# Kernel optimization log

Measured on AMD Instinct MI355X. Metric: run time of the kernel, lower is better.

Reference implementation:

```python
import jax, jax.numpy as jnp
import numpy as np

NUM_LEVELS = 4
SEARCH_RADIUS = 4
EPS = 1e-12  # torch F.normalize eps


def _avg_pool2d(x, s):
    # avg pool with kernel=stride=s over last two dims (exact, since H,W divisible by s)
    lead = x.shape[:-2]
    H, W = x.shape[-2], x.shape[-1]
    x = x.reshape(*lead, H // s, s, W // s, s)
    return x.mean(axis=(-3, -1))


def _l2_normalize(x, axis):
    n = jnp.sqrt(jnp.sum(x * x, axis=axis, keepdims=True))
    return x / jnp.maximum(n, EPS)


def _compute_correlation(query, values, radius):
    # query: [B,C,H,W], values: [B,N,C,H,W] -> [B,N,H,W,(2r+1)^2]
    q = _l2_normalize(query, axis=1)
    v = _l2_normalize(values, axis=2)
    corrs = []
    for dy in range(-radius, radius + 1):
        for dx in range(-radius, radius + 1):
            vs = v if (dy == 0 and dx == 0) else jnp.roll(v, (dy, dx), axis=(-2, -1))
            corrs.append(jnp.einsum('bchw,bnchw->bnhw', q, vs))
    return jnp.stack(corrs, axis=-1)


def setup_inputs() -> dict:
    key = jax.random.key(0)
    k1, k2, k3, k4 = jax.random.split(key, 4)
    B, N, C, H, W = 2, 4, 128, 160, 160
    Co = C // 2
    return {
        'query_feat': jax.random.normal(k1, (B, C, H, W), dtype=jnp.float32),
        'value_feats': jax.random.normal(k2, (B, N, C, H, W), dtype=jnp.float32),
        'proj_w': jax.random.normal(k3, (Co, C), dtype=jnp.float32) * (1.0 / np.sqrt(C)),
        'proj_b': jax.random.normal(k4, (Co,), dtype=jnp.float32) * 0.01,
    }


def reference(query_feat, value_feats, proj_w, proj_b):
    # 1x1 conv projection C -> C//2
    q = jnp.einsum('oc,bchw->bohw', proj_w, query_feat) + proj_b[None, :, None, None]
    v = jnp.einsum('oc,bnchw->bnohw', proj_w, value_feats) + proj_b[None, None, :, None, None]
    outs = []
    for level in range(NUM_LEVELS):
        scale = 2 ** level
        radius = max(1, SEARCH_RADIUS // scale)
        if scale > 1:
            q_l = _avg_pool2d(q, scale)
            v_l = _avg_pool2d(v, scale)
        else:
            q_l, v_l = q, v
        outs.append(_compute_correlation(q_l, v_l, radius))
    return tuple(outs)
```

## Files before the change

### kernel.cpp

```cpp
#include <hip/hip_runtime.h>


typedef _Float16 f16;
typedef _Float16 f16x4 __attribute__((ext_vector_type(4)));
typedef _Float16 f16x8 __attribute__((ext_vector_type(8)));
typedef float f32x4 __attribute__((ext_vector_type(4)));

#define EPSN 1e-12f

__global__ __launch_bounds__(256) void prep_weights(
    const float* __restrict__ wt, f16* __restrict__ wh) {
  int gid = blockIdx.x * 256 + threadIdx.x;
  float4 w = *(const float4*)(wt + gid * 4);
  f16x4 h;
  h[0] = (f16)w.x; h[1] = (f16)w.y; h[2] = (f16)w.z; h[3] = (f16)w.w;
  *(f16x4*)(wh + gid * 4) = h;
}

#define LROW 68
#define WS 136

__global__ __launch_bounds__(256, 3) void proj_pool(
    const float* __restrict__ xq, const float* __restrict__ xv,
    const f16* __restrict__ wh, const float* __restrict__ bias,
    f16* __restrict__ h0, f16* __restrict__ h1,
    f16* __restrict__ h2, f16* __restrict__ h3, int P) {
  __shared__ float xs[128 * LROW];
  __shared__ f16 wsh[64 * WS];
  float* accbuf = (float*)wsh;
  float* l3buf = xs;

  int pb = blockIdx.x;
  int bid = (pb & 7) * 500 + (pb >> 3);

  int img = bid / 400;
  int t = bid - img * 400;
  int ty = t / 20, tx = t - ty * 20;
  int py0 = ty * 8, px0 = tx * 8;
  const float* xsrc = (img < 2) ? (xq + (size_t)img * 128 * P)
                                : (xv + (size_t)(img - 2) * 128 * P);

  int tid = threadIdx.x;
  int lane = tid & 63;
  int wv = tid >> 6;
  int cl = lane & 15;
  int quad = lane >> 4;

  for (int m = tid; m < 1024; m += 256) {
    int o = m >> 4, kk = (m & 15) * 8;
    *(f16x8*)(wsh + o * WS + kk) = *(const f16x8*)(wh + o * 128 + kk);
  }

  {
    int cb = tid >> 4;
    int sub = tid & 15;
    int row = sub >> 1, hf = sub & 1;
#pragma unroll
    for (int i = 0; i < 8; ++i) {
      int c = cb + 16 * i;
      float4 v = *(const float4*)(xsrc + (size_t)c * P + (py0 + row) * 160 + px0 + hf * 4);
      int p = row * 8 + hf * 4;
      int x = (p + 8 * ((c >> 3) & 3)) & 63;
      *(float4*)(xs + c * LROW + x) = v;
    }
  }
  __syncthreads();

  f32x4 acc[4];
#pragma unroll
  for (int m = 0; m < 4; ++m) acc[m] = (f32x4)0.f;

  int pxl = wv * 16 + cl;
  int xr = (pxl + 8 * quad) & 63;

#pragma unroll
  for (int kc = 0; kc < 4; ++kc) {
    f16x8 bfr;
#pragma unroll
    for (int k = 0; k < 8; ++k) {
      int c = kc * 32 + quad * 8 + k;
      bfr[k] = (f16)xs[c * LROW + xr];
    }
    f16x8 afr[4];
#pragma unroll
    for (int mt = 0; mt < 4; ++mt)
      afr[mt] = *(const f16x8*)(wsh + (mt * 16 + cl) * WS + kc * 32 + quad * 8);
#pragma unroll
    for (int mt = 0; mt < 4; ++mt)
      acc[mt] = __builtin_amdgcn_mfma_f32_16x16x32_f16(afr[mt], bfr, acc[mt], 0, 0, 0);
  }

  float4 bi[4];
#pragma unroll
  for (int mt = 0; mt < 4; ++mt) bi[mt] = *(const float4*)(bias + mt * 16 + quad * 4);

  __syncthreads();

  float ss = 0.f;
#pragma unroll
  for (int mt = 0; mt < 4; ++mt) {
    acc[mt][0] += bi[mt].x;
    acc[mt][1] += bi[mt].y;
    acc[mt][2] += bi[mt].z;
    acc[mt][3] += bi[mt].w;
    *(float4*)(accbuf + pxl * LROW + mt * 16 + quad * 4) =
        make_float4(acc[mt][0], acc[mt][1], acc[mt][2], acc[mt][3]);
#pragma unroll
    for (int r = 0; r < 4; ++r) ss = fmaf(acc[mt][r], acc[mt][r], ss);
  }
  ss += __shfl_xor(ss, 16, 64);
  ss += __shfl_xor(ss, 32, 64);
  float s = 1.0f / fmaxf(sqrtf(ss), EPSN);
  {
    int gp = (py0 + (pxl >> 3)) * 160 + px0 + (pxl & 7);
    size_t base = ((size_t)img * P + gp) * 64;
#pragma unroll
    for (int mt = 0; mt < 4; ++mt) {
      f16x4 hn;
      hn[0] = (f16)(acc[mt][0] * s);
      hn[1] = (f16)(acc[mt][1] * s);
      hn[2] = (f16)(acc[mt][2] * s);
      hn[3] = (f16)(acc[mt][3] * s);
      *(f16x4*)(h0 + base + mt * 16 + quad * 4) = hn;
    }
  }
  __syncthreads();

  int r2 = wv >> 1, c2 = wv & 1;
  int g = quad, c4 = cl;
  int r1 = 2 * r2 + (g >> 1), c1 = 2 * c2 + (g & 1);
  int p00 = (2 * r1) * 8 + 2 * c1;

  float4 s00 = *(const float4*)(accbuf + p00 * LROW + c4 * 4);
  float4 s01 = *(const float4*)(accbuf + (p00 + 1) * LROW + c4 * 4);
  float4 s10 = *(const float4*)(accbuf + (p00 + 8) * LROW + c4 * 4);
  float4 s11 = *(const float4*)(accbuf + (p00 + 9) * LROW + c4 * 4);
  float4 v1;
  v1.x = 0.25f * (s00.x + s01.x + s10.x + s11.x);
  v1.y = 0.25f * (s00.y + s01.y + s10.y + s11.y);
  v1.z = 0.25f * (s00.z + s01.z + s10.z + s11.z);
  v1.w = 0.25f * (s00.w + s01.w + s10.w + s11.w);

  {
    float s1 = fmaf(v1.x, v1.x, fmaf(v1.y, v1.y, fmaf(v1.z, v1.z, v1.w * v1.w)));
    s1 += __shfl_xor(s1, 1, 64);
    s1 += __shfl_xor(s1, 2, 64);
    s1 += __shfl_xor(s1, 4, 64);
    s1 += __shfl_xor(s1, 8, 64);
    float sc = 1.0f / fmaxf(sqrtf(s1), EPSN);
    f16x4 h;
    h[0] = (f16)(v1.x * sc); h[1] = (f16)(v1.y * sc);
    h[2] = (f16)(v1.z * sc); h[3] = (f16)(v1.w * sc);
    *(f16x4*)(h1 + ((size_t)(img * 80 + ty * 4 + r1) * 80 + tx * 4 + c1) * 64 + c4 * 4) = h;
  }

  float4 q2v;
  q2v.x = v1.x + __shfl_xor(v1.x, 16, 64);
  q2v.y = v1.y + __shfl_xor(v1.y, 16, 64);
  q2v.z = v1.z + __shfl_xor(v1.z, 16, 64);
  q2v.w = v1.w + __shfl_xor(v1.w, 16, 64);
  q2v.x += __shfl_xor(q2v.x, 32, 64);
  q2v.y += __shfl_xor(q2v.y, 32, 64);
  q2v.z += __shfl_xor(q2v.z, 32, 64);
  q2v.w += __shfl_xor(q2v.w, 32, 64);
  q2v.x *= 0.25f; q2v.y *= 0.25f; q2v.z *= 0.25f; q2v.w *= 0.25f;

  {
    float s2 = fmaf(q2v.x, q2v.x, fmaf(q2v.y, q2v.y, fmaf(q2v.z, q2v.z, q2v.w * q2v.w)));
    s2 += __shfl_xor(s2, 1, 64);
    s2 += __shfl_xor(s2, 2, 64);
    s2 += __shfl_xor(s2, 4, 64);
    s2 += __shfl_xor(s2, 8, 64);
    float sc = 1.0f / fmaxf(sqrtf(s2), EPSN);
    if (g == 0) {
      f16x4 h;
      h[0] = (f16)(q2v.x * sc); h[1] = (f16)(q2v.y * sc);
      h[2] = (f16)(q2v.z * sc); h[3] = (f16)(q2v.w * sc);
      *(f16x4*)(h2 + ((size_t)(img * 40 + ty * 2 + r2) * 40 + tx * 2 + c2) * 64 + c4 * 4) = h;
      *(float4*)(l3buf + (wv * 16 + c4) * 4) = q2v;
    }
  }
  __syncthreads();

  if (tid < 16) {
    float4 a0 = *(const float4*)(l3buf + (0 * 16 + tid) * 4);
    float4 a1 = *(const float4*)(l3buf + (1 * 16 + tid) * 4);
    float4 a2 = *(const float4*)(l3buf + (2 * 16 + tid) * 4);
    float4 a3 = *(const float4*)(l3buf + (3 * 16 + tid) * 4);
    float4 q3;
    q3.x = 0.25f * (a0.x + a1.x + a2.x + a3.x);
    q3.y = 0.25f * (a0.y + a1.y + a2.y + a3.y);
    q3.z = 0.25f * (a0.z + a1.z + a2.z + a3.z);
    q3.w = 0.25f * (a0.w + a1.w + a2.w + a3.w);
    float s3 = fmaf(q3.x, q3.x, fmaf(q3.y, q3.y, fmaf(q3.z, q3.z, q3.w * q3.w)));
    s3 += __shfl_xor(s3, 1, 64);
    s3 += __shfl_xor(s3, 2, 64);
    s3 += __shfl_xor(s3, 4, 64);
    s3 += __shfl_xor(s3, 8, 64);
    float sc = 1.0f / fmaxf(sqrtf(s3), EPSN);
    f16x4 h;
    h[0] = (f16)(q3.x * sc); h[1] = (f16)(q3.y * sc);
    h[2] = (f16)(q3.z * sc); h[3] = (f16)(q3.w * sc);
    *(f16x4*)(h3 + ((size_t)(img * 20 + ty) * 20 + tx) * 64 + tid * 4) = h;
  }
}

template <int R>
__device__ __forceinline__ void corr_level(
    const f16* __restrict__ qh, const f16* __restrict__ vh,
    float* __restrict__ out, int H, int W, int T, int blk, float* lw) {
  constexpr int D = 2 * R + 1, DD = D * D;
  constexpr int PS = (DD + 3) & ~3;
  int bn = blk & 7;
  int wv = threadIdx.x >> 6;
  int widx = (blk >> 3) * 4 + wv;
  int h = widx / T;
  int wt = widx - h * T;
  int lane = threadIdx.x & 63;
  int cl = lane & 15, quad = lane >> 4;
  int b = bn >> 2;
  int w0 = wt * 16;
  float* lwv = lw + wv * 16 * PS;

  int ap = w0 + cl; if (ap >= W) ap = W - 1;
  const f16* qp = qh + ((size_t)(b * H + h) * W + ap) * 64 + quad * 8;
  f16x8 a0 = *(const f16x8*)qp;
  f16x8 a1 = *(const f16x8*)(qp + 32);

  int c0 = w0 - R + cl; if (c0 < 0) c0 += W; if (c0 >= W) c0 -= W;
  int c1 = w0 + R + cl; if (c1 >= W) c1 -= W;
  int b0off = c0 * 64 + quad * 8;
  int b1off = c1 * 64 + quad * 8;

  int rbase = quad * 4;
  int base_dxi = rbase - cl + ((quad < 2) ? 2 * R : 0);

  for (int dyi = 0; dyi < D; ++dyi) {
    int h2 = h - dyi + R; if (h2 < 0) h2 += H; else if (h2 >= H) h2 -= H;
    const f16* vrow = vh + ((size_t)(bn * H + h2) * W) * 64;
    f16x8 b0a = *(const f16x8*)(vrow + b0off);
    f16x8 b0b = *(const f16x8*)(vrow + b0off + 32);
    f16x8 b1a = *(const f16x8*)(vrow + b1off);
    f16x8 b1b = *(const f16x8*)(vrow + b1off + 32);
    f32x4 A0 = __builtin_amdgcn_mfma_f32_16x16x32_f16(a0, b0a, (f32x4)0.f, 0, 0, 0);
    A0 = __builtin_amdgcn_mfma_f32_16x16x32_f16(a1, b0b, A0, 0, 0, 0);
    f32x4 A1 = __builtin_amdgcn_mfma_f32_16x16x32_f16(a0, b1a, (f32x4)0.f, 0, 0, 0);
    A1 = __builtin_amdgcn_mfma_f32_16x16x32_f16(a1, b1b, A1, 0, 0, 0);
#pragma unroll
    for (int rr = 0; rr < 4; ++rr) {
      int dxi = base_dxi + rr;
      float val = (quad < 2) ? A0[rr] : A1[rr];
      if ((unsigned)dxi <= (unsigned)(2 * R))
        lwv[(rbase + rr) * PS + dyi * D + dxi] = val;
    }
  }

  int vp = W - w0; if (vp > 16) vp = 16;
  float* ob = out + ((size_t)(bn * H + h) * W + w0) * DD;
  int tot = vp * DD;
  for (int gg = lane; gg < tot; gg += 64) {
    int pl = gg / DD;
    int rem = gg - pl * DD;
    ob[gg] = lwv[pl * PS + rem];
  }
}

__global__ __launch_bounds__(256, 6) void corr_all(
    const f16* __restrict__ q0, const f16* __restrict__ v0,
    const f16* __restrict__ q1, const f16* __restrict__ v1,
    const f16* __restrict__ q2, const f16* __restrict__ v2,
    const f16* __restrict__ q3, const f16* __restrict__ v3,
    float* __restrict__ o0, float* __restrict__ o1,
    float* __restrict__ o2, float* __restrict__ o3) {
  __shared__ float lw[4 * 16 * 84];
  int blk = blockIdx.x;
  if (blk < 3200)      corr_level<4>(q0, v0, o0, 160, 160, 10, blk, lw);
  else if (blk < 4000) corr_level<2>(q1, v1, o1, 80, 80, 5, blk - 3200, lw);
  else if (blk < 4240) corr_level<1>(q2, v2, o2, 40, 40, 3, blk - 4000, lw);
  else                 corr_level<1>(q3, v3, o3, 20, 20, 2, blk - 4240, lw);
}

extern "C" void kernel_launch(void* const* d_in, const int* in_sizes, int n_in,
                              void* d_out, int out_size, void* d_ws, size_t ws_size,
                              hipStream_t stream) {
  const float* query  = (const float*)d_in[0];
  const float* values = (const float*)d_in[1];
  const float* pw     = (const float*)d_in[2];
  const float* pb     = (const float*)d_in[3];
  float* out = (float*)d_out;
  float* ws  = (float*)d_ws;

  const int B = 2, N = 4;
  const int P0 = 160 * 160;

  f16* h0 = (f16*)ws;
  f16* h1 = h0 + (size_t)10 * P0 * 64;
  f16* h2 = h1 + (size_t)10 * (P0 / 4) * 64;
  f16* h3 = h2 + (size_t)10 * (P0 / 16) * 64;
  f16* wh = h3 + (size_t)10 * (P0 / 64) * 64;

  f16* q0h = h0;             f16* v0h = h0 + (size_t)2 * P0 * 64;
  f16* qh1 = h1;             f16* vh1 = h1 + (size_t)2 * (P0 / 4) * 64;
  f16* qh2 = h2;             f16* vh2 = h2 + (size_t)2 * (P0 / 16) * 64;
  f16* qh3 = h3;             f16* vh3 = h3 + (size_t)2 * (P0 / 64) * 64;

  prep_weights<<<8, 256, 0, stream>>>(pw, wh);

  proj_pool<<<4000, 256, 0, stream>>>(query, values, wh, pb, h0, h1, h2, h3, P0);

  float* out0 = out;
  float* out1 = out0 + (size_t)B * N * P0 * 81;
  float* out2 = out1 + (size_t)B * N * (P0 / 4) * 25;
  float* out3 = out2 + (size_t)B * N * (P0 / 16) * 9;
  corr_all<<<4320, 256, 0, stream>>>(q0h, v0h, qh1, vh1, qh2, vh2, qh3, vh3,
                                     out0, out1, out2, out3);
}
```

Before: 287.4 us.

## Split input transpose to fp16 NHWC into separate kernel before projection

Adds a to_nhwc kernel that converts the fp32 NCHW query and value features into an fp16 channels-last buffer in workspace, using a swizzled shared-memory transpose. proj_pool then loads its MFMA B fragments straight from global memory, drops the large fp32 shared tile and raises its occupancy hint from 3 to 6 blocks. The goal is to remove per-element LDS conversion and free shared memory. In exchange it adds a kernel launch plus a full write and re-read of an fp16 copy of the inputs.

```diff
diff --git a/kernel.cpp b/kernel.cpp
--- a/kernel.cpp
+++ b/kernel.cpp
@@ -17,18 +17,57 @@
   *(f16x4*)(wh + gid * 4) = h;
 }
 
+__global__ __launch_bounds__(256, 4) void to_nhwc(
+    const float* __restrict__ xq, const float* __restrict__ xv,
+    f16* __restrict__ xo, int P) {
+  __shared__ f16 ls[64 * 136];
+
+  int pb = blockIdx.x;
+  int bid = (pb & 7) * 500 + (pb >> 3);
+  int img = bid / 400;
+  int poff = (bid - img * 400) * 64;
+  const float* src = (img < 2) ? (xq + (size_t)img * 128 * P)
+                               : (xv + (size_t)(img - 2) * 128 * P);
+
+  int tid = threadIdx.x;
+  int c0 = tid >> 4;
+  int px4 = (tid & 15) * 4;
+  int swz = ((px4 >> 2) & 7) << 4;
+#pragma unroll
+  for (int i = 0; i < 8; ++i) {
+    int c = c0 + 16 * i;
+    float4 v = *(const float4*)(src + (size_t)c * P + poff + px4);
+    int cx = c ^ swz;
+    ls[(px4 + 0) * 136 + cx] = (f16)v.x;
+    ls[(px4 + 1) * 136 + cx] = (f16)v.y;
+    ls[(px4 + 2) * 136 + cx] = (f16)v.z;
+    ls[(px4 + 3) * 136 + cx] = (f16)v.w;
+  }
+  __syncthreads();
+
+  size_t ob = ((size_t)img * P + poff) * 128;
+#pragma unroll
+  for (int j = 0; j < 4; ++j) {
+    int m = tid + 256 * j;
+    int px = m >> 4;
+    int c8 = (m & 15) * 8;
+    int cx8 = c8 ^ (((px >> 2) & 7) << 4);
+    f16x8 h = *(const f16x8*)(ls + px * 136 + cx8);
+    *(f16x8*)(xo + ob + (size_t)px * 128 + c8) = h;
+  }
+}
+
 #define LROW 68
 #define WS 136
 
-__global__ __launch_bounds__(256, 3) void proj_pool(
-    const float* __restrict__ xq, const float* __restrict__ xv,
-    const f16* __restrict__ wh, const float* __restrict__ bias,
+__global__ __launch_bounds__(256, 6) void proj_pool(
+    const f16* __restrict__ xh, const f16* __restrict__ wh,
+    const float* __restrict__ bias,
     f16* __restrict__ h0, f16* __restrict__ h1,
     f16* __restrict__ h2, f16* __restrict__ h3, int P) {
-  __shared__ float xs[128 * LROW];
   __shared__ f16 wsh[64 * WS];
+  __shared__ float l3buf[64 * 4];
   float* accbuf = (float*)wsh;
-  float* l3buf = xs;
 
   int pb = blockIdx.x;
   int bid = (pb & 7) * 500 + (pb >> 3);
@@ -37,8 +76,6 @@
   int t = bid - img * 400;
   int ty = t / 20, tx = t - ty * 20;
   int py0 = ty * 8, px0 = tx * 8;
-  const float* xsrc = (img < 2) ? (xq + (size_t)img * 128 * P)
-                                : (xv + (size_t)(img - 2) * 128 * P);
 
   int tid = threadIdx.x;
   int lane = tid & 63;
@@ -51,43 +88,28 @@
     *(f16x8*)(wsh + o * WS + kk) = *(const f16x8*)(wh + o * 128 + kk);
   }
 
-  {
-    int cb = tid >> 4;
-    int sub = tid & 15;
-    int row = sub >> 1, hf = sub & 1;
-#pragma unroll
-    for (int i = 0; i < 8; ++i) {
-      int c = cb + 16 * i;
-      float4 v = *(const float4*)(xsrc + (size_t)c * P + (py0 + row) * 160 + px0 + hf * 4);
-      int p = row * 8 + hf * 4;
-      int x = (p + 8 * ((c >> 3) & 3)) & 63;
-      *(float4*)(xs + c * LROW + x) = v;
-    }
-  }
+  int pxl = wv * 16 + cl;
+  int gp = (py0 + (pxl >> 3)) * 160 + px0 + (pxl & 7);
+  const f16* xp = xh + ((size_t)img * P + gp) * 128 + quad * 8;
+  f16x8 bfr[4];
+#pragma unroll
+  for (int kc = 0; kc < 4; ++kc) bfr[kc] = *(const f16x8*)(xp + kc * 32);
+
   __syncthreads();
 
   f32x4 acc[4];
 #pragma unroll
   for (int m = 0; m < 4; ++m) acc[m] = (f32x4)0.f;
 
-  int pxl = wv * 16 + cl;
-  int xr = (pxl + 8 * quad) & 63;
-
 #pragma unroll
   for (int kc = 0; kc < 4; ++kc) {
-    f16x8 bfr;
-#pragma unroll
-    for (int k = 0; k < 8; ++k) {
-      int c = kc * 32 + quad * 8 + k;
-      bfr[k] = (f16)xs[c * LROW + xr];
-    }
     f16x8 afr[4];
 #pragma unroll
     for (int mt = 0; mt < 4; ++mt)
       afr[mt] = *(const f16x8*)(wsh + (mt * 16 + cl) * WS + kc * 32 + quad * 8);
 #pragma unroll
     for (int mt = 0; mt < 4; ++mt)
-      acc[mt] = __builtin_amdgcn_mfma_f32_16x16x32_f16(afr[mt], bfr, acc[mt], 0, 0, 0);
+      acc[mt] = __builtin_amdgcn_mfma_f32_16x16x32_f16(afr[mt], bfr[kc], acc[mt], 0, 0, 0);
   }
 
   float4 bi[4];
@@ -112,7 +134,6 @@
   ss += __shfl_xor(ss, 32, 64);
   float s = 1.0f / fmaxf(sqrtf(ss), EPSN);
   {
-    int gp = (py0 + (pxl >> 3)) * 160 + px0 + (pxl & 7);
     size_t base = ((size_t)img * P + gp) * 64;
 #pragma unroll
     for (int mt = 0; mt < 4; ++mt) {
@@ -298,6 +319,7 @@
   f16* h2 = h1 + (size_t)10 * (P0 / 4) * 64;
   f16* h3 = h2 + (size_t)10 * (P0 / 16) * 64;
   f16* wh = h3 + (size_t)10 * (P0 / 64) * 64;
+  f16* xh = wh + 8192;
 
   f16* q0h = h0;             f16* v0h = h0 + (size_t)2 * P0 * 64;
   f16* qh1 = h1;             f16* vh1 = h1 + (size_t)2 * (P0 / 4) * 64;
@@ -306,7 +328,9 @@
 
   prep_weights<<<8, 256, 0, stream>>>(pw, wh);
 
-  proj_pool<<<4000, 256, 0, stream>>>(query, values, wh, pb, h0, h1, h2, h3, P0);
+  to_nhwc<<<4000, 256, 0, stream>>>(query, values, xh, P0);
+
+  proj_pool<<<4000, 256, 0, stream>>>(xh, wh, pb, h0, h1, h2, h3, P0);
 
   float* out0 = out;
   float* out1 = out0 + (size_t)B * N * P0 * 81;
```

Measured after the change: 299.0 us. 4.1% more time.
